# Kernel tuning notes

Measured on AMD Instinct MI355X. Metric: run time of the kernel, lower is better.

The kernel has to match this reference:

```python
import jax, jax.numpy as jnp
import numpy as np

S, B, IN, HID, H, D, DFF, L, NC, EMB = 1024, 32, 3072, 256, 16, 16, 1024, 4, 1623, 10


def setup_inputs() -> dict:
    key = jax.random.key(0)
    ks = jax.random.split(key, 12)
    w = lambda k, shp: 0.02 * jax.random.normal(k, shp, dtype=jnp.float32)
    return {
        "x": jax.random.normal(ks[0], (S, B, IN), dtype=jnp.float32),
        "fb": jax.random.randint(ks[1], (S, B), 0, NC),
        "fc1_w": w(ks[2], (HID, IN)),
        "fc1_b": jnp.zeros((HID,), jnp.float32),
        "emb": w(ks[3], (NC, EMB)),
        "proj_w": w(ks[4], (HID, HID + EMB)),
        "proj_b": jnp.zeros((HID,), jnp.float32),
        "ln1_g": jnp.ones((L, HID), jnp.float32),
        "ln1_b": jnp.zeros((L, HID), jnp.float32),
        "slow_w": w(ks[5], (L, H * (3 * D + 1), HID)),
        "out_w": w(ks[6], (L, HID, H * D)),
        "ln2_g": jnp.ones((L, HID), jnp.float32),
        "ln2_b": jnp.zeros((L, HID), jnp.float32),
        "ff1_w": w(ks[7], (L, DFF, HID)),
        "ff1_b": jnp.zeros((L, DFF), jnp.float32),
        "ff2_w": w(ks[8], (L, HID, DFF)),
        "ff2_b": jnp.zeros((L, HID), jnp.float32),
        "outl_w": w(ks[9], (NC, HID)),
        "outl_b": jnp.zeros((NC,), jnp.float32),
    }


def _ln(x, g, b):
    m = jnp.mean(x, -1, keepdims=True)
    v = jnp.mean(jnp.square(x - m), -1, keepdims=True)
    return (x - m) * jax.lax.rsqrt(v + 1e-5) * g + b


def _delta_attn(x, g, b, sw, ow):
    # x: (S, B, HID); delta-rule fast-weight linear attention
    s, bsz, _ = x.shape
    qkvb = jnp.einsum('sbi,oi->sbo', _ln(x, g, b), sw).reshape(s, bsz, H, 3 * D + 1)
    q, k, v, beta = jnp.split(qkvb, [D, 2 * D, 3 * D], axis=-1)
    q = jax.nn.softmax(q, axis=-1)      # sum-normalized feature map
    k = jax.nn.softmax(k, axis=-1)
    beta = jax.nn.sigmoid(beta)         # (S,B,H,1)

    def step(W, inp):
        qt, kt, vt, bt = inp            # (B,H,D),(B,H,D),(B,H,D),(B,H,1)
        v_old = jnp.einsum('bhkv,bhk->bhv', W, kt)
        v_new = bt * vt + (1.0 - bt) * v_old
        W = W + jnp.einsum('bhk,bhv->bhkv', kt, v_new - v_old)
        return W, jnp.einsum('bhkv,bhk->bhv', W, qt)

    W0 = jnp.zeros((bsz, H, D, D), x.dtype)
    _, o = jax.lax.scan(step, W0, (q, k, v, beta))   # o: (S,B,H,D)
    return x + jnp.einsum('sbi,oi->sbo', o.reshape(s, bsz, H * D), ow)


def _ffn(x, g, b, w1, b1, w2, b2):
    h = jax.nn.relu(jnp.einsum('sbi,oi->sbo', _ln(x, g, b), w1) + b1)
    return x + jnp.einsum('sbi,oi->sbo', h, w2) + b2


def reference(x, fb, fc1_w, fc1_b, emb, proj_w, proj_b, ln1_g, ln1_b, slow_w,
              out_w, ln2_g, ln2_b, ff1_w, ff1_b, ff2_w, ff2_b, outl_w, outl_b):
    h = jnp.einsum('sbi,oi->sbo', x, fc1_w) + fc1_b
    h = jnp.concatenate([h, emb[fb]], axis=-1)
    h = jnp.einsum('sbi,oi->sbo', h, proj_w) + proj_b
    for l in range(L):
        h = _delta_attn(h, ln1_g[l], ln1_b[l], slow_w[l], out_w[l])
        h = _ffn(h, ln2_g[l], ln2_b[l], ff1_w[l], ff1_b[l], ff2_w[l], ff2_b[l])
    return jnp.einsum('sbi,oi->sbo', h, outl_w) + outl_b
```

## Files before the change

kernel.cpp:

```cpp
#include <hip/hip_runtime.h>
#include <hip/hip_bf16.h>

#define S_LEN  1024
#define B_SZ   32
#define IN_DIM 3072
#define HID    256
#define NHEAD  16
#define HDIM   16
#define DFF    1024
#define NLAYER 4
#define NCLS   1623
#define EMB_D  10
#define MROWS  (S_LEN * B_SZ)
#define QSTRIDE 52

using bf16   = __hip_bfloat16;
using short8 = __attribute__((ext_vector_type(8))) short;
using f32x4  = __attribute__((ext_vector_type(4))) float;

#define GLOAD16(g, l) __builtin_amdgcn_global_load_lds(                        \
    (const __attribute__((address_space(1))) void*)(g),                        \
    (__attribute__((address_space(3))) void*)(l), 16, 0, 0)

template<int FLAGS>
__global__ __launch_bounds__(256) void mgemm(
    const bf16* __restrict__ A, const bf16* __restrict__ W,
    const float* __restrict__ bias, void* C, int N, int K, int Wld)
{
    __shared__ bf16 sA[2][128 * 32];
    __shared__ bf16 sB[2][128 * 32];
    const int t    = threadIdx.x;
    const int lane = t & 63;
    const int wid  = t >> 6;
    const int wr   = wid >> 1, wc = wid & 1;
    const long bm  = (long)blockIdx.x * 128;
    const int  bn  = blockIdx.y * 128;
    const int  fr  = lane & 15;
    const int  fg  = lane >> 4;
    const int  row0 = t >> 2;
    const int  kq0  = (t & 3) << 3;

    f32x4 acc[4][4];
#pragma unroll
    for (int m = 0; m < 4; ++m)
#pragma unroll
        for (int n = 0; n < 4; ++n)
#pragma unroll
            for (int r = 0; r < 4; ++r) acc[m][n][r] = 0.f;

    const int nkt = K >> 5;

    auto stage = [&](int buf, int kt) {
        const int k0 = kt << 5;
        GLOAD16(A + (bm + row0)      * (long)K   + k0 + kq0, &sA[buf][(t      ) * 8]);
        GLOAD16(A + (bm + row0 + 64) * (long)K   + k0 + kq0, &sA[buf][(t + 256) * 8]);
        GLOAD16(W + (long)(bn + row0)      * Wld + k0 + kq0, &sB[buf][(t      ) * 8]);
        GLOAD16(W + (long)(bn + row0 + 64) * Wld + k0 + kq0, &sB[buf][(t + 256) * 8]);
    };

    stage(0, 0);
    __syncthreads();
    for (int kt = 0; kt < nkt; ++kt) {
        const int cur = kt & 1;
        if (kt + 1 < nkt) stage(cur ^ 1, kt + 1);
        short8 af[4], bg[4];
#pragma unroll
        for (int m = 0; m < 4; ++m)
            af[m] = *(const short8*)&sA[cur][(wr * 64 + m * 16 + fr) * 32 + fg * 8];
#pragma unroll
        for (int n = 0; n < 4; ++n)
            bg[n] = *(const short8*)&sB[cur][(wc * 64 + n * 16 + fr) * 32 + fg * 8];
#pragma unroll
        for (int m = 0; m < 4; ++m)
#pragma unroll
            for (int n = 0; n < 4; ++n)
                acc[m][n] = __builtin_amdgcn_mfma_f32_16x16x32_bf16(
                    af[m], bg[n], acc[m][n], 0, 0, 0);
        __syncthreads();
    }

    float bs[4];
#pragma unroll
    for (int n = 0; n < 4; ++n) {
        const int c = bn + wc * 64 + n * 16 + fr;
        bs[n] = ((FLAGS & 1) && c < N) ? bias[c] : 0.f;
    }
#pragma unroll
    for (int m = 0; m < 4; ++m) {
#pragma unroll
        for (int n = 0; n < 4; ++n) {
            const int c = bn + wc * 64 + n * 16 + fr;
            if (c < N) {
#pragma unroll
                for (int r = 0; r < 4; ++r) {
                    const long rw = bm + wr * 64 + m * 16 + fg * 4 + r;
                    float v = acc[m][n][r] + bs[n];
                    if (FLAGS & 2) v = fmaxf(v, 0.f);
                    if (FLAGS & 16) {
                        const int s = (int)(rw >> 5), b = (int)(rw & 31);
                        const int hh = c / 49, cc = c - hh * 49;
                        ((float*)C)[((long)(b * 16 + hh) * 1024 + s) * QSTRIDE + cc] = v;
                    } else if (FLAGS & 8) {
                        ((bf16*)C)[rw * N + c] = __float2bfloat16(v);
                    } else {
                        ((float*)C)[rw * N + c] = v;
                    }
                }
            }
        }
    }
}

template<int FLAGS>
__global__ __launch_bounds__(256) void gemm_ln(
    const bf16* __restrict__ A, const bf16* __restrict__ W,
    const float* __restrict__ bias, const float* __restrict__ lg,
    const float* __restrict__ lb, float* H, bf16* __restrict__ Y, int K)
{
    __shared__ bf16 sA[2][64 * 32];
    __shared__ bf16 sB[2][256 * 32];
    __shared__ float rsum[64][4];
    __shared__ float rsq[64][4];
    const int t    = threadIdx.x;
    const int lane = t & 63;
    const int w    = t >> 6;
    const int fr   = lane & 15;
    const int fg   = lane >> 4;
    const long bm  = (long)blockIdx.x * 64;

    f32x4 acc[4][4];
#pragma unroll
    for (int m = 0; m < 4; ++m)
#pragma unroll
        for (int n = 0; n < 4; ++n)
#pragma unroll
            for (int r = 0; r < 4; ++r) acc[m][n][r] = 0.f;

    const int nkt = K >> 5;
    auto stage = [&](int buf, int kt) {
        const int k0 = kt << 5;
        GLOAD16(A + (bm + (t >> 2)) * (long)K + k0 + ((t & 3) << 3),
                &sA[buf][t * 8]);
#pragma unroll
        for (int i = 0; i < 4; ++i)
            GLOAD16(W + (long)((i << 6) + (t >> 2)) * K + k0 + ((t & 3) << 3),
                    &sB[buf][(i * 256 + t) * 8]);
    };

    stage(0, 0);
    __syncthreads();
    for (int kt = 0; kt < nkt; ++kt) {
        const int cur = kt & 1;
        if (kt + 1 < nkt) stage(cur ^ 1, kt + 1);
        short8 af[4], bg[4];
#pragma unroll
        for (int m = 0; m < 4; ++m)
            af[m] = *(const short8*)&sA[cur][(m * 16 + fr) * 32 + fg * 8];
#pragma unroll
        for (int n = 0; n < 4; ++n)
            bg[n] = *(const short8*)&sB[cur][(w * 64 + n * 16 + fr) * 32 + fg * 8];
#pragma unroll
        for (int m = 0; m < 4; ++m)
#pragma unroll
            for (int n = 0; n < 4; ++n)
                acc[m][n] = __builtin_amdgcn_mfma_f32_16x16x32_bf16(
                    af[m], bg[n], acc[m][n], 0, 0, 0);
        __syncthreads();
    }

    float bs[4];
#pragma unroll
    for (int n = 0; n < 4; ++n) {
        const int c = w * 64 + n * 16 + fr;
        bs[n] = (FLAGS & 1) ? bias[c] : 0.f;
    }
    float ps[4][4], pq[4][4];
#pragma unroll
    for (int m = 0; m < 4; ++m)
#pragma unroll
        for (int r = 0; r < 4; ++r) { ps[m][r] = 0.f; pq[m][r] = 0.f; }
#pragma unroll
    for (int m = 0; m < 4; ++m)
#pragma unroll
        for (int n = 0; n < 4; ++n)
#pragma unroll
            for (int r = 0; r < 4; ++r) {
                const long rw = bm + m * 16 + fg * 4 + r;
                const int c = w * 64 + n * 16 + fr;
                float v = acc[m][n][r] + bs[n];
                if (FLAGS & 4) v += H[rw * HID + c];
                H[rw * HID + c] = v;
                acc[m][n][r] = v;
                ps[m][r] += v;
                pq[m][r] += v * v;
            }
    if (FLAGS & 8) {
#pragma unroll
        for (int m = 0; m < 4; ++m)
#pragma unroll
            for (int n = 0; n < 4; ++n)
#pragma unroll
                for (int r = 0; r < 4; ++r) {
                    const long rw = bm + m * 16 + fg * 4 + r;
                    const int c = w * 64 + n * 16 + fr;
                    Y[rw * HID + c] = __float2bfloat16(acc[m][n][r]);
                }
    } else {
#pragma unroll
        for (int m = 0; m < 4; ++m)
#pragma unroll
            for (int r = 0; r < 4; ++r) {
                float s = ps[m][r], q = pq[m][r];
                s += __shfl_xor(s, 1); q += __shfl_xor(q, 1);
                s += __shfl_xor(s, 2); q += __shfl_xor(q, 2);
                s += __shfl_xor(s, 4); q += __shfl_xor(q, 4);
                s += __shfl_xor(s, 8); q += __shfl_xor(q, 8);
                ps[m][r] = s; pq[m][r] = q;
            }
        if (fr == 0) {
#pragma unroll
            for (int m = 0; m < 4; ++m)
#pragma unroll
                for (int r = 0; r < 4; ++r) {
                    const int row = m * 16 + fg * 4 + r;
                    rsum[row][w] = ps[m][r];
                    rsq[row][w]  = pq[m][r];
                }
        }
        __syncthreads();
#pragma unroll
        for (int m = 0; m < 4; ++m)
#pragma unroll
            for (int r = 0; r < 4; ++r) {
                const int row = m * 16 + fg * 4 + r;
                const float4 s4 = *(const float4*)&rsum[row][0];
                const float4 q4 = *(const float4*)&rsq[row][0];
                const float S = (s4.x + s4.y) + (s4.z + s4.w);
                const float Q = (q4.x + q4.y) + (q4.z + q4.w);
                const float mean = S * (1.f / 256.f);
                const float inv  = rsqrtf(Q * (1.f / 256.f) - mean * mean + 1e-5f);
                const long rw = bm + row;
#pragma unroll
                for (int n = 0; n < 4; ++n) {
                    const int c = w * 64 + n * 16 + fr;
                    const float y = (acc[m][n][r] - mean) * inv * lg[c] + lb[c];
                    Y[rw * HID + c] = __float2bfloat16(y);
                }
            }
    }
}

__global__ __launch_bounds__(256) void fc1_k(
    const float* __restrict__ A, const bf16* __restrict__ W,
    const float* __restrict__ bias, bf16* __restrict__ hcat)
{
    __shared__ bf16 sA[2][128 * 32];
    __shared__ bf16 sB[2][128 * 32];
    const int t    = threadIdx.x;
    const int lane = t & 63;
    const int wid  = t >> 6;
    const int wr   = wid >> 1, wc = wid & 1;
    const long bm  = (long)blockIdx.x * 128;
    const int  bn  = blockIdx.y * 128;
    const int  fr  = lane & 15;
    const int  fg  = lane >> 4;
    const int  row0 = t >> 2;
    const int  kq0  = (t & 3) << 3;
    const int  arow = t >> 3;
    const int  ac4  = (t & 7) << 2;

    f32x4 acc[4][4];
#pragma unroll
    for (int m = 0; m < 4; ++m)
#pragma unroll
        for (int n = 0; n < 4; ++n)
#pragma unroll
            for (int r = 0; r < 4; ++r) acc[m][n][r] = 0.f;

    auto stageB = [&](int buf, int kt) {
        const int k0 = kt << 5;
        GLOAD16(W + (long)(bn + row0)      * IN_DIM + k0 + kq0, &sB[buf][(t      ) * 8]);
        GLOAD16(W + (long)(bn + row0 + 64) * IN_DIM + k0 + kq0, &sB[buf][(t + 256) * 8]);
    };
    float4 va[4];
    auto loadA = [&](int kt) {
        const int k0 = kt << 5;
#pragma unroll
        for (int rep = 0; rep < 4; ++rep)
            va[rep] = *(const float4*)(A + (bm + arow + rep * 32) * (long)IN_DIM + k0 + ac4);
    };
    auto writeA = [&](int buf) {
#pragma unroll
        for (int rep = 0; rep < 4; ++rep) {
            alignas(8) bf16 tb[4];
            tb[0] = __float2bfloat16(va[rep].x);
            tb[1] = __float2bfloat16(va[rep].y);
            tb[2] = __float2bfloat16(va[rep].z);
            tb[3] = __float2bfloat16(va[rep].w);
            *(ushort4*)&sA[buf][(arow + rep * 32) * 32 + ac4] = *(const ushort4*)tb;
        }
    };

    loadA(0);
    stageB(0, 0);
    writeA(0);
    __syncthreads();
    const int nkt = IN_DIM >> 5;
    for (int kt = 0; kt < nkt; ++kt) {
        const int cur = kt & 1;
        if (kt + 1 < nkt) { stageB(cur ^ 1, kt + 1); loadA(kt + 1); }
        short8 af[4], bg[4];
#pragma unroll
        for (int m = 0; m < 4; ++m)
            af[m] = *(const short8*)&sA[cur][(wr * 64 + m * 16 + fr) * 32 + fg * 8];
#pragma unroll
        for (int n = 0; n < 4; ++n)
            bg[n] = *(const short8*)&sB[cur][(wc * 64 + n * 16 + fr) * 32 + fg * 8];
#pragma unroll
        for (int m = 0; m < 4; ++m)
#pragma unroll
            for (int n = 0; n < 4; ++n)
                acc[m][n] = __builtin_amdgcn_mfma_f32_16x16x32_bf16(
                    af[m], bg[n], acc[m][n], 0, 0, 0);
        if (kt + 1 < nkt) writeA(cur ^ 1);
        __syncthreads();
    }

#pragma unroll
    for (int n = 0; n < 4; ++n) {
        const int c = bn + wc * 64 + n * 16 + fr;
        const float bsn = bias[c];
#pragma unroll
        for (int m = 0; m < 4; ++m)
#pragma unroll
            for (int r = 0; r < 4; ++r) {
                const long rw = bm + wr * 64 + m * 16 + fg * 4 + r;
                hcat[rw * 288 + c] = __float2bfloat16(acc[m][n][r] + bsn);
            }
    }
}

__global__ __launch_bounds__(256) void fillemb(
    const float* __restrict__ emb, const int* __restrict__ fb,
    bf16* __restrict__ hcat)
{
    const long row = (long)blockIdx.x * 8 + (threadIdx.x >> 5);
    const int c = threadIdx.x & 31;
    bf16 v = (c < EMB_D) ? __float2bfloat16(emb[(long)fb[row] * EMB_D + c])
                         : __float2bfloat16(0.f);
    hcat[row * 288 + 256 + c] = v;
}

__global__ __launch_bounds__(256) void cvt8(const float* __restrict__ s,
                                            bf16* __restrict__ d, long n8)
{
    for (long i = (long)blockIdx.x * 256 + threadIdx.x; i < n8;
         i += (long)gridDim.x * 256) {
        const float4 a = ((const float4*)s)[i * 2];
        const float4 b = ((const float4*)s)[i * 2 + 1];
        alignas(16) bf16 t[8];
        t[0] = __float2bfloat16(a.x); t[1] = __float2bfloat16(a.y);
        t[2] = __float2bfloat16(a.z); t[3] = __float2bfloat16(a.w);
        t[4] = __float2bfloat16(b.x); t[5] = __float2bfloat16(b.y);
        t[6] = __float2bfloat16(b.z); t[7] = __float2bfloat16(b.w);
        ((short8*)d)[i] = *(const short8*)t;
    }
}

__global__ __launch_bounds__(256) void cvtpad(const float* __restrict__ s,
                                              bf16* __restrict__ d,
                                              int rows, int cols, int prows, int pcols)
{
    const long tot = (long)prows * pcols;
    for (long i = (long)blockIdx.x * 256 + threadIdx.x; i < tot;
         i += (long)gridDim.x * 256) {
        const int r = (int)(i / pcols), c = (int)(i - (long)r * pcols);
        d[i] = (r < rows && c < cols) ? __float2bfloat16(s[(long)r * cols + c])
                                      : __float2bfloat16(0.f);
    }
}

__global__ __launch_bounds__(256) void cvtpad_slow(const float* __restrict__ s,
                                                   bf16* __restrict__ d)
{
    const int l = blockIdx.y;
    const float* src = s + (size_t)l * 784 * HID;
    bf16* dst = d + (size_t)l * 896 * HID;
    const long tot = (long)896 * HID;
    for (long i = (long)blockIdx.x * 256 + threadIdx.x; i < tot;
         i += (long)gridDim.x * 256) {
        const int r = (int)(i / HID), c = (int)(i - (long)r * HID);
        dst[i] = (r < 784) ? __float2bfloat16(src[(long)r * HID + c])
                           : __float2bfloat16(0.f);
    }
}

#define DOT16(dst, kr, s0, s1, s2, s3) do {                                    \
    float _pa = fmaf(kr[3],  (s0).w, fmaf(kr[2],  (s0).z, fmaf(kr[1],  (s0).y, kr[0]  * (s0).x))); \
    float _pb = fmaf(kr[7],  (s1).w, fmaf(kr[6],  (s1).z, fmaf(kr[5],  (s1).y, kr[4]  * (s1).x))); \
    float _pc = fmaf(kr[11], (s2).w, fmaf(kr[10], (s2).z, fmaf(kr[9],  (s2).y, kr[8]  * (s2).x))); \
    float _pd = fmaf(kr[15], (s3).w, fmaf(kr[14], (s3).z, fmaf(kr[13], (s3).y, kr[12] * (s3).x))); \
    dst = (_pa + _pb) + (_pc + _pd);                                           \
} while (0)

__global__ __launch_bounds__(64) void scan9(
    const float* __restrict__ qkvb, bf16* __restrict__ o)
{
    __shared__ float sbuf[2][1792];
    __shared__ float W0l[16 * 20];
    __shared__ float DVl[16 * 20];
    const int lane = threadIdx.x;
    const int i4 = lane >> 2;
    const int jq = lane & 3;
    const int chain = blockIdx.x;
    const int b = chain >> 4, hh = chain & 15;
    const float* cb = qkvb + (long)chain * S_LEN * QSTRIDE;
    bf16* po = o + (long)b * HID + hh * HDIM + jq * 4;

    for (int z = lane; z < 320; z += 64) W0l[z] = 0.f;

    auto stage = [&](int buf, int nb2) {
#pragma unroll
        for (int iss = 0; iss < 7; ++iss) {
            const float* src = cb + (long)nb2 * 1664 + iss * 256 + lane * 4;
            GLOAD16(src, &sbuf[buf][iss * 256 + lane * 4]);
        }
    };

    stage(0, 0);
    asm volatile("s_waitcnt vmcnt(0)" ::: "memory");
    for (int nb = 0; nb < 32; ++nb) {
        const int buf = nb & 1;
        asm volatile("s_waitcnt vmcnt(2)" ::: "memory");
        if (nb + 1 < 32) stage(buf ^ 1, nb + 1);

        float* sb = sbuf[buf];
        {
            float* p = sb + (lane >> 1) * 52 + ((lane & 1) << 4);
            float4 a0 = *(float4*)(p),     a1 = *(float4*)(p + 4);
            float4 a2 = *(float4*)(p + 8), a3 = *(float4*)(p + 12);
            float mx = fmaxf(fmaxf(fmaxf(a0.x, a0.y), fmaxf(a0.z, a0.w)),
                             fmaxf(fmaxf(a1.x, a1.y), fmaxf(a1.z, a1.w)));
            mx = fmaxf(mx, fmaxf(fmaxf(fmaxf(a2.x, a2.y), fmaxf(a2.z, a2.w)),
                                 fmaxf(fmaxf(a3.x, a3.y), fmaxf(a3.z, a3.w))));
            a0.x = __expf(a0.x - mx); a0.y = __expf(a0.y - mx);
            a0.z = __expf(a0.z - mx); a0.w = __expf(a0.w - mx);
            a1.x = __expf(a1.x - mx); a1.y = __expf(a1.y - mx);
            a1.z = __expf(a1.z - mx); a1.w = __expf(a1.w - mx);
            a2.x = __expf(a2.x - mx); a2.y = __expf(a2.y - mx);
            a2.z = __expf(a2.z - mx); a2.w = __expf(a2.w - mx);
            a3.x = __expf(a3.x - mx); a3.y = __expf(a3.y - mx);
            a3.z = __expf(a3.z - mx); a3.w = __expf(a3.w - mx);
            const float sum = ((a0.x + a0.y) + (a0.z + a0.w))
                            + ((a1.x + a1.y) + (a1.z + a1.w))
                            + ((a2.x + a2.y) + (a2.z + a2.w))
                            + ((a3.x + a3.y) + (a3.z + a3.w));
            const float inv = 1.f / sum;
            a0.x *= inv; a0.y *= inv; a0.z *= inv; a0.w *= inv;
            a1.x *= inv; a1.y *= inv; a1.z *= inv; a1.w *= inv;
            a2.x *= inv; a2.y *= inv; a2.z *= inv; a2.w *= inv;
            a3.x *= inv; a3.y *= inv; a3.z *= inv; a3.w *= inv;
            *(float4*)(p)      = a0; *(float4*)(p + 4)  = a1;
            *(float4*)(p + 8)  = a2; *(float4*)(p + 12) = a3;
            if (!(lane & 1)) p[48] = 1.f / (1.f + __expf(-p[48]));
        }
        asm volatile("s_waitcnt lgkmcnt(0)" ::: "memory");

#pragma unroll
        for (int t = 0; t < 2; ++t) {
            const float* rb = sb + t * 16 * 52;
            const float* myrow = rb + i4 * 52;
            float ki[16], qi[16];
            {
                const float4 kA = *(const float4*)(myrow + 16);
                const float4 kB = *(const float4*)(myrow + 20);
                const float4 kC = *(const float4*)(myrow + 24);
                const float4 kD = *(const float4*)(myrow + 28);
                ki[0]=kA.x; ki[1]=kA.y; ki[2]=kA.z; ki[3]=kA.w;
                ki[4]=kB.x; ki[5]=kB.y; ki[6]=kB.z; ki[7]=kB.w;
                ki[8]=kC.x; ki[9]=kC.y; ki[10]=kC.z; ki[11]=kC.w;
                ki[12]=kD.x; ki[13]=kD.y; ki[14]=kD.z; ki[15]=kD.w;
                const float4 qA = *(const float4*)(myrow);
                const float4 qB = *(const float4*)(myrow + 4);
                const float4 qC = *(const float4*)(myrow + 8);
                const float4 qD = *(const float4*)(myrow + 12);
                qi[0]=qA.x; qi[1]=qA.y; qi[2]=qA.z; qi[3]=qA.w;
                qi[4]=qB.x; qi[5]=qB.y; qi[6]=qB.z; qi[7]=qB.w;
                qi[8]=qC.x; qi[9]=qC.y; qi[10]=qC.z; qi[11]=qC.w;
                qi[12]=qD.x; qi[13]=qD.y; qi[14]=qD.z; qi[15]=qD.w;
            }
            const float beta = myrow[48];
            float gcf[4], qkc[4];
#pragma unroll
            for (int m = 0; m < 4; ++m) {
                const int s = jq * 4 + m;
                const float* sr = rb + s * 52 + 16;
                const float4 s0 = *(const float4*)(sr);
                const float4 s1 = *(const float4*)(sr + 4);
                const float4 s2 = *(const float4*)(sr + 8);
                const float4 s3 = *(const float4*)(sr + 12);
                float g, qk;
                DOT16(g, ki, s0, s1, s2, s3);
                DOT16(qk, qi, s0, s1, s2, s3);
                gcf[m] = (s < i4)  ? -beta * g : 0.f;
                qkc[m] = (s <= i4) ? qk : 0.f;
            }
            float P0=0,P1=0,P2=0,P3=0, O0=0,O1=0,O2=0,O3=0;
#pragma unroll
            for (int x = 0; x < 16; ++x) {
                const float4 w = *(const float4*)&W0l[x * 20 + jq * 4];
                P0 = fmaf(ki[x], w.x, P0); P1 = fmaf(ki[x], w.y, P1);
                P2 = fmaf(ki[x], w.z, P2); P3 = fmaf(ki[x], w.w, P3);
                O0 = fmaf(qi[x], w.x, O0); O1 = fmaf(qi[x], w.y, O1);
                O2 = fmaf(qi[x], w.z, O2); O3 = fmaf(qi[x], w.w, O3);
            }
            const float4 vv = *(const float4*)(myrow + 32 + jq * 4);
            float d0 = beta * (vv.x - P0), d1 = beta * (vv.y - P1);
            float d2 = beta * (vv.z - P2), d3 = beta * (vv.w - P3);
#pragma unroll
            for (int s = 0; s < 15; ++s) {
                const float cf = __shfl(gcf[s & 3], i4 * 4 + (s >> 2));
                const float e0 = __shfl(d0, s * 4 + jq);
                const float e1 = __shfl(d1, s * 4 + jq);
                const float e2 = __shfl(d2, s * 4 + jq);
                const float e3 = __shfl(d3, s * 4 + jq);
                d0 = fmaf(cf, e0, d0); d1 = fmaf(cf, e1, d1);
                d2 = fmaf(cf, e2, d2); d3 = fmaf(cf, e3, d3);
            }
            f32x4 dvv; dvv[0]=d0; dvv[1]=d1; dvv[2]=d2; dvv[3]=d3;
            *(f32x4*)&DVl[i4 * 20 + jq * 4] = dvv;
            asm volatile("s_waitcnt lgkmcnt(0)" ::: "memory");
            float a0=0,a1=0,a2=0,a3=0;
#pragma unroll
            for (int s = 0; s < 16; ++s) {
                const float4 dvs = *(const float4*)&DVl[s * 20 + jq * 4];
                const float cqk = __shfl(qkc[s & 3], i4 * 4 + (s >> 2));
                O0 = fmaf(cqk, dvs.x, O0); O1 = fmaf(cqk, dvs.y, O1);
                O2 = fmaf(cqk, dvs.z, O2); O3 = fmaf(cqk, dvs.w, O3);
                const float kx = rb[s * 52 + 16 + i4];
                a0 = fmaf(kx, dvs.x, a0); a1 = fmaf(kx, dvs.y, a1);
                a2 = fmaf(kx, dvs.z, a2); a3 = fmaf(kx, dvs.w, a3);
            }
            {
                const int sg = nb * 32 + t * 16 + i4;
                alignas(8) bf16 tb[4];
                tb[0] = __float2bfloat16(O0); tb[1] = __float2bfloat16(O1);
                tb[2] = __float2bfloat16(O2); tb[3] = __float2bfloat16(O3);
                *(ushort4*)((unsigned short*)(po + (long)sg * (B_SZ * HID))) =
                    *(const ushort4*)tb;
            }
            {
                float4 w = *(const float4*)&W0l[i4 * 20 + jq * 4];
                w.x += a0; w.y += a1; w.z += a2; w.w += a3;
                *(float4*)&W0l[i4 * 20 + jq * 4] = w;
            }
            asm volatile("s_waitcnt lgkmcnt(0)" ::: "memory");
        }
    }
}

extern "C" void kernel_launch(void* const* d_in, const int* in_sizes, int n_in,
                              void* d_out, int out_size, void* d_ws, size_t ws_size,
                              hipStream_t stream)
{
    const float* x      = (const float*)d_in[0];
    const int*   fb     = (const int*)  d_in[1];
    const float* fc1_w  = (const float*)d_in[2];
    const float* fc1_b  = (const float*)d_in[3];
    const float* emb    = (const float*)d_in[4];
    const float* proj_w = (const float*)d_in[5];
    const float* proj_b = (const float*)d_in[6];
    const float* ln1_g  = (const float*)d_in[7];
    const float* ln1_b  = (const float*)d_in[8];
    const float* slow_w = (const float*)d_in[9];
    const float* out_w  = (const float*)d_in[10];
    const float* ln2_g  = (const float*)d_in[11];
    const float* ln2_b  = (const float*)d_in[12];
    const float* ff1_w  = (const float*)d_in[13];
    const float* ff1_b  = (const float*)d_in[14];
    const float* ff2_w  = (const float*)d_in[15];
    const float* ff2_b  = (const float*)d_in[16];
    const float* outl_w = (const float*)d_in[17];
    const float* outl_b = (const float*)d_in[18];

    char* wp = (char*)d_ws;
    float* h    = (float*)wp;                 wp += (size_t)MROWS * HID * 4;
    bf16*  abuf = (bf16*)wp;                  wp += (size_t)MROWS * HID * 2;
    bf16*  fc1b = (bf16*)wp;                  wp += (size_t)HID * IN_DIM * 2;
    bf16*  projb= (bf16*)wp;                  wp += (size_t)HID * 288 * 2;
    bf16*  slowb= (bf16*)wp;                  wp += (size_t)NLAYER * 896 * HID * 2;
    bf16*  outwb= (bf16*)wp;                  wp += (size_t)NLAYER * HID * HID * 2;
    bf16*  ff1b = (bf16*)wp;                  wp += (size_t)NLAYER * DFF * HID * 2;
    bf16*  ff2b = (bf16*)wp;                  wp += (size_t)NLAYER * HID * DFF * 2;
    bf16*  outlb= (bf16*)wp;                  wp += (size_t)1664 * HID * 2;

    bf16*  hcat = (bf16*)d_out;
    float* qkvb = (float*)d_out;
    bf16*  hff  = (bf16*)d_out;

    const dim3 blk(256);

    cvt8<<<dim3(384),  blk, 0, stream>>>(fc1_w, fc1b, (long)HID * IN_DIM / 8);
    cvtpad<<<dim3(288), blk, 0, stream>>>(proj_w, projb, HID, HID + EMB_D, HID, 288);
    cvtpad_slow<<<dim3(896, 4), blk, 0, stream>>>(slow_w, slowb);
    cvt8<<<dim3(128), blk, 0, stream>>>(out_w, outwb, (long)NLAYER * HID * HID / 8);
    cvt8<<<dim3(512), blk, 0, stream>>>(ff1_w, ff1b, (long)NLAYER * DFF * HID / 8);
    cvt8<<<dim3(512), blk, 0, stream>>>(ff2_w, ff2b, (long)NLAYER * HID * DFF / 8);
    cvtpad<<<dim3(1664), blk, 0, stream>>>(outl_w, outlb, NCLS, HID, 1664, HID);

    fc1_k<<<dim3(256, 2), blk, 0, stream>>>(x, fc1b, fc1_b, hcat);
    fillemb<<<dim3(MROWS / 8), blk, 0, stream>>>(emb, fb, hcat);
    gemm_ln<1><<<dim3(512), blk, 0, stream>>>(hcat, projb, proj_b,
                                              ln1_g, ln1_b, h, abuf, 288);

    for (int l = 0; l < NLAYER; ++l) {
        mgemm<16><<<dim3(256, 7), blk, 0, stream>>>(abuf, slowb + (size_t)l * 896 * HID,
                                                    nullptr, qkvb, 784, HID, HID);
        scan9<<<dim3(B_SZ * NHEAD), dim3(64), 0, stream>>>(qkvb, abuf);
        gemm_ln<4><<<dim3(512), blk, 0, stream>>>(abuf, outwb + (size_t)l * HID * HID,
                                                  nullptr, ln2_g + l * HID,
                                                  ln2_b + l * HID, h, abuf, HID);
        mgemm<11><<<dim3(256, 8), blk, 0, stream>>>(abuf, ff1b + (size_t)l * DFF * HID,
                                                    ff1_b + l * DFF, hff, DFF, HID, HID);
        if (l + 1 < NLAYER)
            gemm_ln<5><<<dim3(512), blk, 0, stream>>>(hff, ff2b + (size_t)l * HID * DFF,
                                                      ff2_b + l * HID,
                                                      ln1_g + (l + 1) * HID,
                                                      ln1_b + (l + 1) * HID, h, abuf, DFF);
        else
            gemm_ln<13><<<dim3(512), blk, 0, stream>>>(hff, ff2b + (size_t)l * HID * DFF,
                                                       ff2_b + l * HID,
                                                       nullptr, nullptr, h, abuf, DFF);
    }
    mgemm<1><<<dim3(256, 13), blk, 0, stream>>>(abuf, outlb, outl_b, d_out,
                                                NCLS, HID, HID);
}
```

Baseline: 1.626 ms.

## Store qkvb intermediate in bf16, fuse beta sigmoid into GEMM, merge weight conversions

The QKV-beta projection GEMM now writes bf16 instead of fp32 into a per-chain layout with row stride 56, and applies the beta sigmoid in its epilogue. The scan kernel stages half as many bytes per chunk and unpacks bf16 into an fp32 LDS work buffer before the recurrence. The seven weight-conversion launches are merged into one flat kernel. This is meant to cut memory traffic between the projection and the scan plus launch overhead, at the cost of bf16 rounding on q, k, v and beta, an extra LDS pass in the scan, and a scalar, branchy conversion loop.

```diff
diff --git a/kernel.cpp b/kernel.cpp
--- a/kernel.cpp
+++ b/kernel.cpp
@@ -12,7 +12,7 @@
 #define NCLS   1623
 #define EMB_D  10
 #define MROWS  (S_LEN * B_SZ)
-#define QSTRIDE 52
+#define QROW   56
 
 using bf16   = __hip_bfloat16;
 using short8 = __attribute__((ext_vector_type(8))) short;
@@ -21,6 +21,12 @@
 #define GLOAD16(g, l) __builtin_amdgcn_global_load_lds(                        \
     (const __attribute__((address_space(1))) void*)(g),                        \
     (__attribute__((address_space(3))) void*)(l), 16, 0, 0)
+
+__device__ __forceinline__ float b2f(short s) {
+    union { float f; unsigned u; } x;
+    x.u = ((unsigned)(unsigned short)s) << 16;
+    return x.f;
+}
 
 template<int FLAGS>
 __global__ __launch_bounds__(256) void mgemm(
@@ -99,7 +105,9 @@
                     if (FLAGS & 16) {
                         const int s = (int)(rw >> 5), b = (int)(rw & 31);
                         const int hh = c / 49, cc = c - hh * 49;
-                        ((float*)C)[((long)(b * 16 + hh) * 1024 + s) * QSTRIDE + cc] = v;
+                        if (cc == 48) v = 1.f / (1.f + __expf(-v));
+                        ((bf16*)C)[((long)(b * 16 + hh) * 1024 + s) * QROW + cc] =
+                            __float2bfloat16(v);
                     } else if (FLAGS & 8) {
                         ((bf16*)C)[rw * N + c] = __float2bfloat16(v);
                     } else {
@@ -351,47 +359,39 @@
     hcat[row * 288 + 256 + c] = v;
 }
 
-__global__ __launch_bounds__(256) void cvt8(const float* __restrict__ s,
-                                            bf16* __restrict__ d, long n8)
+__global__ __launch_bounds__(256) void cvtall(
+    const float* __restrict__ fc1_w, const float* __restrict__ proj_w,
+    const float* __restrict__ slow_w, const float* __restrict__ out_w,
+    const float* __restrict__ ff1_w, const float* __restrict__ ff2_w,
+    const float* __restrict__ outl_w, bf16* __restrict__ dst)
 {
-    for (long i = (long)blockIdx.x * 256 + threadIdx.x; i < n8;
+    for (long i = (long)blockIdx.x * 256 + threadIdx.x; i < 4562944L;
          i += (long)gridDim.x * 256) {
-        const float4 a = ((const float4*)s)[i * 2];
-        const float4 b = ((const float4*)s)[i * 2 + 1];
-        alignas(16) bf16 t[8];
-        t[0] = __float2bfloat16(a.x); t[1] = __float2bfloat16(a.y);
-        t[2] = __float2bfloat16(a.z); t[3] = __float2bfloat16(a.w);
-        t[4] = __float2bfloat16(b.x); t[5] = __float2bfloat16(b.y);
-        t[6] = __float2bfloat16(b.z); t[7] = __float2bfloat16(b.w);
-        ((short8*)d)[i] = *(const short8*)t;
-    }
-}
-
-__global__ __launch_bounds__(256) void cvtpad(const float* __restrict__ s,
-                                              bf16* __restrict__ d,
-                                              int rows, int cols, int prows, int pcols)
-{
-    const long tot = (long)prows * pcols;
-    for (long i = (long)blockIdx.x * 256 + threadIdx.x; i < tot;
-         i += (long)gridDim.x * 256) {
-        const int r = (int)(i / pcols), c = (int)(i - (long)r * pcols);
-        d[i] = (r < rows && c < cols) ? __float2bfloat16(s[(long)r * cols + c])
-                                      : __float2bfloat16(0.f);
-    }
-}
-
-__global__ __launch_bounds__(256) void cvtpad_slow(const float* __restrict__ s,
-                                                   bf16* __restrict__ d)
-{
-    const int l = blockIdx.y;
-    const float* src = s + (size_t)l * 784 * HID;
-    bf16* dst = d + (size_t)l * 896 * HID;
-    const long tot = (long)896 * HID;
-    for (long i = (long)blockIdx.x * 256 + threadIdx.x; i < tot;
-         i += (long)gridDim.x * 256) {
-        const int r = (int)(i / HID), c = (int)(i - (long)r * HID);
-        dst[i] = (r < 784) ? __float2bfloat16(src[(long)r * HID + c])
-                           : __float2bfloat16(0.f);
+        float v;
+        if (i < 786432L) {
+            v = fc1_w[i];
+        } else if (i < 860160L) {
+            const long j = i - 786432L;
+            const int r = (int)(j / 288), c = (int)(j - (long)r * 288);
+            v = (c < 266) ? proj_w[(long)r * 266 + c] : 0.f;
+        } else if (i < 1777664L) {
+            const long j = i - 860160L;
+            const int l = (int)(j / 229376);
+            const long m = j - (long)l * 229376;
+            const int r = (int)(m >> 8), c = (int)(m & 255);
+            v = (r < 784) ? slow_w[(long)l * 200704 + (long)r * 256 + c] : 0.f;
+        } else if (i < 2039808L) {
+            v = out_w[i - 1777664L];
+        } else if (i < 3088384L) {
+            v = ff1_w[i - 2039808L];
+        } else if (i < 4136960L) {
+            v = ff2_w[i - 3088384L];
+        } else {
+            const long j = i - 4136960L;
+            const int r = (int)(j >> 8), c = (int)(j & 255);
+            v = (r < 1623) ? outl_w[(long)r * 256 + c] : 0.f;
+        }
+        dst[i] = __float2bfloat16(v);
     }
 }
 
@@ -403,10 +403,11 @@
     dst = (_pa + _pb) + (_pc + _pd);                                           \
 } while (0)
 
-__global__ __launch_bounds__(64) void scan9(
-    const float* __restrict__ qkvb, bf16* __restrict__ o)
+__global__ __launch_bounds__(64) void scan10(
+    const bf16* __restrict__ qkvb, bf16* __restrict__ o)
 {
-    __shared__ float sbuf[2][1792];
+    __shared__ short sbf[2][2048];
+    __shared__ float wrk[32 * 52];
     __shared__ float W0l[16 * 20];
     __shared__ float DVl[16 * 20];
     const int lane = threadIdx.x;
@@ -414,16 +415,16 @@
     const int jq = lane & 3;
     const int chain = blockIdx.x;
     const int b = chain >> 4, hh = chain & 15;
-    const float* cb = qkvb + (long)chain * S_LEN * QSTRIDE;
+    const char* cbb = (const char*)(qkvb + (long)chain * S_LEN * QROW);
     bf16* po = o + (long)b * HID + hh * HDIM + jq * 4;
 
     for (int z = lane; z < 320; z += 64) W0l[z] = 0.f;
 
     auto stage = [&](int buf, int nb2) {
 #pragma unroll
-        for (int iss = 0; iss < 7; ++iss) {
-            const float* src = cb + (long)nb2 * 1664 + iss * 256 + lane * 4;
-            GLOAD16(src, &sbuf[buf][iss * 256 + lane * 4]);
+        for (int iss = 0; iss < 4; ++iss) {
+            const char* src = cbb + (long)nb2 * 3584 + (iss * 64 + lane) * 16;
+            GLOAD16(src, &sbf[buf][(iss * 64 + lane) * 8]);
         }
     };
 
@@ -434,41 +435,36 @@
         asm volatile("s_waitcnt vmcnt(2)" ::: "memory");
         if (nb + 1 < 32) stage(buf ^ 1, nb + 1);
 
-        float* sb = sbuf[buf];
         {
-            float* p = sb + (lane >> 1) * 52 + ((lane & 1) << 4);
-            float4 a0 = *(float4*)(p),     a1 = *(float4*)(p + 4);
-            float4 a2 = *(float4*)(p + 8), a3 = *(float4*)(p + 12);
-            float mx = fmaxf(fmaxf(fmaxf(a0.x, a0.y), fmaxf(a0.z, a0.w)),
-                             fmaxf(fmaxf(a1.x, a1.y), fmaxf(a1.z, a1.w)));
-            mx = fmaxf(mx, fmaxf(fmaxf(fmaxf(a2.x, a2.y), fmaxf(a2.z, a2.w)),
-                                 fmaxf(fmaxf(a3.x, a3.y), fmaxf(a3.z, a3.w))));
-            a0.x = __expf(a0.x - mx); a0.y = __expf(a0.y - mx);
-            a0.z = __expf(a0.z - mx); a0.w = __expf(a0.w - mx);
-            a1.x = __expf(a1.x - mx); a1.y = __expf(a1.y - mx);
-            a1.z = __expf(a1.z - mx); a1.w = __expf(a1.w - mx);
-            a2.x = __expf(a2.x - mx); a2.y = __expf(a2.y - mx);
-            a2.z = __expf(a2.z - mx); a2.w = __expf(a2.w - mx);
-            a3.x = __expf(a3.x - mx); a3.y = __expf(a3.y - mx);
-            a3.z = __expf(a3.z - mx); a3.w = __expf(a3.w - mx);
-            const float sum = ((a0.x + a0.y) + (a0.z + a0.w))
-                            + ((a1.x + a1.y) + (a1.z + a1.w))
-                            + ((a2.x + a2.y) + (a2.z + a2.w))
-                            + ((a3.x + a3.y) + (a3.z + a3.w));
+            const int row = lane >> 1, hf = lane & 1;
+            const short* ps = &sbf[buf][row * QROW + hf * 16];
+            const short8 r0 = *(const short8*)(ps);
+            const short8 r1 = *(const short8*)(ps + 8);
+            float f[16];
+#pragma unroll
+            for (int j = 0; j < 8; ++j) { f[j] = b2f(r0[j]); f[8 + j] = b2f(r1[j]); }
+            float mx = f[0];
+#pragma unroll
+            for (int j = 1; j < 16; ++j) mx = fmaxf(mx, f[j]);
+            float sum = 0.f;
+#pragma unroll
+            for (int j = 0; j < 16; ++j) { f[j] = __expf(f[j] - mx); sum += f[j]; }
             const float inv = 1.f / sum;
-            a0.x *= inv; a0.y *= inv; a0.z *= inv; a0.w *= inv;
-            a1.x *= inv; a1.y *= inv; a1.z *= inv; a1.w *= inv;
-            a2.x *= inv; a2.y *= inv; a2.z *= inv; a2.w *= inv;
-            a3.x *= inv; a3.y *= inv; a3.z *= inv; a3.w *= inv;
-            *(float4*)(p)      = a0; *(float4*)(p + 4)  = a1;
-            *(float4*)(p + 8)  = a2; *(float4*)(p + 12) = a3;
-            if (!(lane & 1)) p[48] = 1.f / (1.f + __expf(-p[48]));
+            float* pw = wrk + row * 52 + hf * 16;
+#pragma unroll
+            for (int j = 0; j < 16; ++j) pw[j] = f[j] * inv;
+            const short8 rv = *(const short8*)(&sbf[buf][row * QROW + 32 + hf * 8]);
+            float* pv = wrk + row * 52 + 32 + hf * 8;
+#pragma unroll
+            for (int j = 0; j < 8; ++j) pv[j] = b2f(rv[j]);
+            if (hf == 0)
+                wrk[row * 52 + 48] = b2f(sbf[buf][row * QROW + 48]);
         }
         asm volatile("s_waitcnt lgkmcnt(0)" ::: "memory");
 
 #pragma unroll
         for (int t = 0; t < 2; ++t) {
-            const float* rb = sb + t * 16 * 52;
+            const float* rb = wrk + t * 16 * 52;
             const float* myrow = rb + i4 * 52;
             float ki[16], qi[16];
             {
@@ -595,18 +591,13 @@
     bf16*  outlb= (bf16*)wp;                  wp += (size_t)1664 * HID * 2;
 
     bf16*  hcat = (bf16*)d_out;
-    float* qkvb = (float*)d_out;
+    bf16*  qkvb = (bf16*)d_out;
     bf16*  hff  = (bf16*)d_out;
 
     const dim3 blk(256);
 
-    cvt8<<<dim3(384),  blk, 0, stream>>>(fc1_w, fc1b, (long)HID * IN_DIM / 8);
-    cvtpad<<<dim3(288), blk, 0, stream>>>(proj_w, projb, HID, HID + EMB_D, HID, 288);
-    cvtpad_slow<<<dim3(896, 4), blk, 0, stream>>>(slow_w, slowb);
-    cvt8<<<dim3(128), blk, 0, stream>>>(out_w, outwb, (long)NLAYER * HID * HID / 8);
-    cvt8<<<dim3(512), blk, 0, stream>>>(ff1_w, ff1b, (long)NLAYER * DFF * HID / 8);
-    cvt8<<<dim3(512), blk, 0, stream>>>(ff2_w, ff2b, (long)NLAYER * HID * DFF / 8);
-    cvtpad<<<dim3(1664), blk, 0, stream>>>(outl_w, outlb, NCLS, HID, 1664, HID);
+    cvtall<<<dim3(1024), blk, 0, stream>>>(fc1_w, proj_w, slow_w, out_w,
+                                           ff1_w, ff2_w, outl_w, fc1b);
 
     fc1_k<<<dim3(256, 2), blk, 0, stream>>>(x, fc1b, fc1_b, hcat);
     fillemb<<<dim3(MROWS / 8), blk, 0, stream>>>(emb, fb, hcat);
@@ -616,7 +607,7 @@
     for (int l = 0; l < NLAYER; ++l) {
         mgemm<16><<<dim3(256, 7), blk, 0, stream>>>(abuf, slowb + (size_t)l * 896 * HID,
                                                     nullptr, qkvb, 784, HID, HID);
-        scan9<<<dim3(B_SZ * NHEAD), dim3(64), 0, stream>>>(qkvb, abuf);
+        scan10<<<dim3(B_SZ * NHEAD), dim3(64), 0, stream>>>(qkvb, abuf);
         gemm_ln<4><<<dim3(512), blk, 0, stream>>>(abuf, outwb + (size_t)l * HID * HID,
                                                   nullptr, ln2_g + l * HID,
                                                   ln2_b + l * HID, h, abuf, HID);
```

New measurement: 1.620 ms. About the same (-0.3%).
